# Performance work log

Measured on AMD Instinct MI355X. Metric: run time of the kernel, lower is better.

## Reference

```python
import jax, jax.numpy as jnp
import numpy as np

EPS = 1e-5

def _rmsnorm(x, g):
    xf = x.astype(jnp.float32)
    rms = jnp.sqrt(jnp.mean(xf * xf + EPS, axis=-1, keepdims=True))
    return (xf / rms * g).astype(x.dtype)

def setup_inputs() -> dict:
    key = jax.random.key(0)
    ks = jax.random.split(key, 10)
    B, S, D, H, F = 2, 2048, 1024, 16, 4096
    s = 0.02
    return {
        "x": jax.random.normal(ks[0], (B, S, D), jnp.float32),
        "g1": jnp.ones((D,), jnp.float32),
        "wq": jax.random.normal(ks[1], (D, D), jnp.float32) * s,
        "wk": jax.random.normal(ks[2], (D, D), jnp.float32) * s,
        "wv": jax.random.normal(ks[3], (D, D), jnp.float32) * s,
        "wo": jax.random.normal(ks[4], (D, D), jnp.float32) * s,
        "g2": jnp.ones((D,), jnp.float32),
        "w1": jax.random.normal(ks[5], (F, D), jnp.float32) * s,
        "w2": jax.random.normal(ks[6], (D, F), jnp.float32) * s,
        "w3": jax.random.normal(ks[7], (F, D), jnp.float32) * s,
    }

def reference(x, g1, wq, wk, wv, wo, g2, w1, w2, w3):
    B, S, D = x.shape
    H = 16
    hd = D // H
    # --- attention sublayer ---
    xn = _rmsnorm(x, g1)
    q = jnp.einsum('bsd,ed->bse', xn, wq).reshape(B, S, H, hd).transpose(0, 2, 1, 3)
    k = jnp.einsum('bsd,ed->bse', xn, wk).reshape(B, S, H, hd).transpose(0, 2, 1, 3)
    v = jnp.einsum('bsd,ed->bse', xn, wv).reshape(B, S, H, hd).transpose(0, 2, 1, 3)
    scores = jnp.einsum('bhqd,bhkd->bhqk', q, k) / jnp.sqrt(jnp.float32(hd))
    mask = jnp.tril(jnp.ones((S, S), bool))  # causal
    neg = jnp.finfo(scores.dtype).min
    scores = jnp.where(mask[None, None], scores, neg)
    probs = jax.nn.softmax(scores, axis=-1)
    o = jnp.einsum('bhqk,bhkd->bhqd', probs, v)
    o = o.transpose(0, 2, 1, 3).reshape(B, S, D)
    attn_out = jnp.einsum('bsv,dv->bsd', o, wo)
    h = x + attn_out
    # --- SwiGLU sublayer ---
    hn = _rmsnorm(h, g2)
    p1 = jnp.einsum('fd,bsd->bsf', w1, hn)
    p3 = jnp.einsum('fd,bsd->bsf', w3, hn)
    ffn = jnp.einsum('df,bsf->bsd', w2, jax.nn.silu(p1) * p3)
    return h + ffn
```

## Files before the change

### kernel.cpp

```cpp
#include <hip/hip_runtime.h>

typedef __attribute__((ext_vector_type(8))) short short8;
typedef __attribute__((ext_vector_type(4))) float f32x4;

__device__ __forceinline__ unsigned short f2b(float f) {
  union { float f; unsigned u; } v; v.f = f;
  unsigned r = v.u + 0x7fffu + ((v.u >> 16) & 1u);
  return (unsigned short)(r >> 16);
}
__device__ __forceinline__ float b2f(unsigned short b) {
  union { unsigned u; float f; } v; v.u = ((unsigned)b) << 16; return v.f;
}

__device__ __forceinline__ void gload_lds16(const void* g, void* l) {
  __builtin_amdgcn_global_load_lds(
      (const __attribute__((address_space(1))) void*)g,
      (__attribute__((address_space(3))) void*)l, 16, 0, 0);
}

__global__ __launch_bounds__(256) void cvt_k(const float* __restrict__ s,
                                             unsigned short* __restrict__ d, int n4) {
  int i = blockIdx.x * 256 + threadIdx.x;
  if (i >= n4) return;
  float4 v = ((const float4*)s)[i];
  ushort4 o;
  o.x = f2b(v.x); o.y = f2b(v.y); o.z = f2b(v.z); o.w = f2b(v.w);
  ((ushort4*)d)[i] = o;
}

__global__ __launch_bounds__(256) void rmsnorm_k(const float* __restrict__ x,
                                                 const float* __restrict__ g,
                                                 unsigned short* __restrict__ out) {
  const int row = blockIdx.x, tid = threadIdx.x;
  const float4 v = ((const float4*)(x + (size_t)row * 1024))[tid];
  float ss = v.x*v.x + v.y*v.y + v.z*v.z + v.w*v.w;
  #pragma unroll
  for (int d = 32; d > 0; d >>= 1) ss += __shfl_down(ss, d);
  __shared__ float red[4];
  if ((tid & 63) == 0) red[tid >> 6] = ss;
  __syncthreads();
  const float tot = red[0] + red[1] + red[2] + red[3];
  const float sc = rsqrtf(tot * (1.0f/1024.0f) + 1e-5f);
  const float4 gg = ((const float4*)g)[tid];
  ushort4 o;
  o.x = f2b(v.x * sc * gg.x); o.y = f2b(v.y * sc * gg.y);
  o.z = f2b(v.z * sc * gg.z); o.w = f2b(v.w * sc * gg.w);
  ((ushort4*)(out + (size_t)row * 1024))[tid] = o;
}

__global__ __launch_bounds__(256) void gate_k(unsigned short* __restrict__ p13) {
  const size_t i = (size_t)blockIdx.x * 256 + threadIdx.x;
  const int r = (int)(i >> 9);
  const int fc = ((int)i & 511) * 8;
  unsigned short* p1 = p13 + (size_t)r * 8192 + fc;
  const unsigned short* p3 = p13 + (size_t)r * 8192 + 4096 + fc;
  ushort4 a0 = ((const ushort4*)p1)[0], a1 = ((const ushort4*)p1)[1];
  ushort4 b0 = ((const ushort4*)p3)[0], b1 = ((const ushort4*)p3)[1];
  unsigned short va[8] = {a0.x,a0.y,a0.z,a0.w,a1.x,a1.y,a1.z,a1.w};
  unsigned short vb[8] = {b0.x,b0.y,b0.z,b0.w,b1.x,b1.y,b1.z,b1.w};
  unsigned short vo[8];
  #pragma unroll
  for (int j = 0; j < 8; ++j) {
    float f1 = b2f(va[j]), f3 = b2f(vb[j]);
    float s = f1 / (1.0f + __expf(-f1));
    vo[j] = f2b(s * f3);
  }
  ushort4 o0 = {vo[0],vo[1],vo[2],vo[3]}, o1 = {vo[4],vo[5],vo[6],vo[7]};
  ((ushort4*)p1)[0] = o0; ((ushort4*)p1)[1] = o1;
}

template<int EPI>
__global__ __launch_bounds__(256) void gemm_bt(
    const unsigned short* __restrict__ A, const unsigned short* __restrict__ W,
    int N, int K, int lda,
    unsigned short* __restrict__ Cb, const float* __restrict__ res,
    float* __restrict__ Cf, int ldc)
{
  __shared__ unsigned short sA[4096];
  __shared__ unsigned short sB[4096];
  const int tid = threadIdx.x;
  const int w = tid >> 6, l = tid & 63;
  const int l15 = l & 15, l4 = l >> 4;
  const int bm = blockIdx.y * 128, bn = blockIdx.x * 128;
  const int wm = (w >> 1) * 64, wn = (w & 1) * 64;
  const int c0 = w * 128 + l;
  const int ra0 = c0 >> 2,        ka0 = (c0 & 3) * 8;
  const int ra1 = (c0 + 64) >> 2, ka1 = ((c0 + 64) & 3) * 8;
  const unsigned short* Ar0 = A + (size_t)(bm + ra0) * lda + ka0;
  const unsigned short* Ar1 = A + (size_t)(bm + ra1) * lda + ka1;
  const unsigned short* Wr0 = W + (size_t)(bn + ra0) * K + ka0;
  const unsigned short* Wr1 = W + (size_t)(bn + ra1) * K + ka1;
  f32x4 acc[4][4];
  const f32x4 z4 = {0.f, 0.f, 0.f, 0.f};
  #pragma unroll
  for (int i = 0; i < 4; ++i)
    #pragma unroll
    for (int j = 0; j < 4; ++j) acc[i][j] = z4;

  for (int kt = 0; kt < K; kt += 32) {
    gload_lds16(Ar0 + kt, &sA[w * 1024]);
    gload_lds16(Ar1 + kt, &sA[w * 1024 + 512]);
    gload_lds16(Wr0 + kt, &sB[w * 1024]);
    gload_lds16(Wr1 + kt, &sB[w * 1024 + 512]);
    __syncthreads();
    short8 af[4], bf[4];
    #pragma unroll
    for (int mi = 0; mi < 4; ++mi)
      af[mi] = *(const short8*)&sA[(wm + mi*16 + l15)*32 + l4*8];
    #pragma unroll
    for (int ni = 0; ni < 4; ++ni)
      bf[ni] = *(const short8*)&sB[(wn + ni*16 + l15)*32 + l4*8];
    #pragma unroll
    for (int mi = 0; mi < 4; ++mi)
      #pragma unroll
      for (int ni = 0; ni < 4; ++ni)
        acc[mi][ni] = __builtin_amdgcn_mfma_f32_16x16x32_bf16(af[mi], bf[ni], acc[mi][ni], 0, 0, 0);
    __syncthreads();
  }
  #pragma unroll
  for (int mi = 0; mi < 4; ++mi)
    #pragma unroll
    for (int ni = 0; ni < 4; ++ni) {
      const int row0 = bm + wm + mi*16 + l4*4;
      const int col  = bn + wn + ni*16 + l15;
      #pragma unroll
      for (int r = 0; r < 4; ++r) {
        const float v = acc[mi][ni][r];
        if (EPI == 0) {
          Cb[(size_t)(row0 + r) * ldc + col] = f2b(v);
        } else {
          const size_t o = (size_t)(row0 + r) * ldc + col;
          Cf[o] = res[o] + v;
        }
      }
    }
}

__global__ __launch_bounds__(512, 2) void gemm256_bt(
    const unsigned short* __restrict__ A, const unsigned short* __restrict__ W,
    int K, int lda, unsigned short* __restrict__ Cb, int ldc, int nbx)
{
  __shared__ unsigned short sA[4][8192];
  __shared__ unsigned short sB[4][8192];
  const int tid = threadIdx.x;
  const int w = tid >> 6, l = tid & 63;
  const int l15 = l & 15, l4 = l >> 4;
  const int nwg = nbx * gridDim.y;
  const int flat = blockIdx.y * nbx + blockIdx.x;
  const int q8 = nwg >> 3;
  const int sw = (flat & 7) * q8 + (flat >> 3);
  const int bm = (sw / nbx) * 256, bn = (sw % nbx) * 256;

  int rowl[2], coll[2];
  #pragma unroll
  for (int i = 0; i < 2; ++i) {
    const int g = w * 128 + i * 64 + l;
    const int s = g >> 6, j = g & 63;
    const int r = j >> 2, c8 = (j & 3) * 8;
    rowl[i] = s * 16 + r;
    coll[i] = c8 ^ ((r & 8) << 1);
  }
  const unsigned short* As0 = A + (size_t)(bm + rowl[0]) * lda + coll[0];
  const unsigned short* As1 = A + (size_t)(bm + rowl[1]) * lda + coll[1];
  const unsigned short* Ws0 = W + (size_t)(bn + rowl[0]) * K + coll[0];
  const unsigned short* Ws1 = W + (size_t)(bn + rowl[1]) * K + coll[1];
  const int d0 = w * 1024, d1 = w * 1024 + 512;

  const int swzr = (l4 * 8) ^ ((l15 & 8) << 1);
  const int aoff = (w >> 2) * 4096 + l15 * 32 + swzr;
  const int boff = (w & 3) * 2048 + l15 * 32 + swzr;

  f32x4 acc[8][4];
  const f32x4 z4 = {0.f, 0.f, 0.f, 0.f};
  #pragma unroll
  for (int i = 0; i < 8; ++i)
    #pragma unroll
    for (int j = 0; j < 4; ++j) acc[i][j] = z4;

  const int NT = K >> 5;
  #pragma unroll
  for (int p = 0; p < 3; ++p) {
    const int ko = p * 32;
    gload_lds16(As0 + ko, &sA[p][d0]);
    gload_lds16(As1 + ko, &sA[p][d1]);
    gload_lds16(Ws0 + ko, &sB[p][d0]);
    gload_lds16(Ws1 + ko, &sB[p][d1]);
  }
  asm volatile("s_waitcnt vmcnt(8)" ::: "memory");
  __builtin_amdgcn_s_barrier();

  for (int t = 0; t < NT; ++t) {
    const unsigned short* a_ = sA[t & 3];
    const unsigned short* b_ = sB[t & 3];
    const bool st = (t + 3 < NT);
    const int nb = (t + 3) & 3;
    const int ko = (t + 3) * 32;
    short8 bfr[4], afr[4];
    #pragma unroll
    for (int ni = 0; ni < 4; ++ni) bfr[ni] = *(const short8*)&b_[boff + ni * 512];
    #pragma unroll
    for (int mi = 0; mi < 4; ++mi) afr[mi] = *(const short8*)&a_[aoff + mi * 512];
    if (st) { gload_lds16(As0 + ko, &sA[nb][d0]); gload_lds16(Ws0 + ko, &sB[nb][d0]); }
    __builtin_amdgcn_s_barrier();
    asm volatile("s_waitcnt lgkmcnt(0)" ::: "memory");
    __builtin_amdgcn_sched_barrier(0);
    __builtin_amdgcn_s_setprio(1);
    #pragma unroll
    for (int mi = 0; mi < 4; ++mi)
      #pragma unroll
      for (int ni = 0; ni < 4; ++ni)
        acc[mi][ni] = __builtin_amdgcn_mfma_f32_16x16x32_bf16(bfr[ni], afr[mi], acc[mi][ni], 0, 0, 0);
    __builtin_amdgcn_s_setprio(0);
    __builtin_amdgcn_s_barrier();
    #pragma unroll
    for (int mi = 0; mi < 4; ++mi) afr[mi] = *(const short8*)&a_[aoff + (mi + 4) * 512];
    if (st) { gload_lds16(As1 + ko, &sA[nb][d1]); gload_lds16(Ws1 + ko, &sB[nb][d1]); }
    __builtin_amdgcn_s_barrier();
    asm volatile("s_waitcnt lgkmcnt(0)" ::: "memory");
    __builtin_amdgcn_sched_barrier(0);
    __builtin_amdgcn_s_setprio(1);
    #pragma unroll
    for (int mi = 0; mi < 4; ++mi)
      #pragma unroll
      for (int ni = 0; ni < 4; ++ni)
        acc[mi + 4][ni] = __builtin_amdgcn_mfma_f32_16x16x32_bf16(bfr[ni], afr[mi], acc[mi + 4][ni], 0, 0, 0);
    __builtin_amdgcn_s_setprio(0);
    if (t < NT - 3)       asm volatile("s_waitcnt vmcnt(8)" ::: "memory");
    else if (t == NT - 3) asm volatile("s_waitcnt vmcnt(4)" ::: "memory");
    else                  asm volatile("s_waitcnt vmcnt(0)" ::: "memory");
    __builtin_amdgcn_s_barrier();
  }
  #pragma unroll
  for (int mi = 0; mi < 8; ++mi) {
    const int row = bm + (w >> 2) * 128 + mi * 16 + l15;
    #pragma unroll
    for (int ni = 0; ni < 4; ++ni) {
      const int col = bn + (w & 3) * 64 + ni * 16 + l4 * 4;
      ushort4 o = { f2b(acc[mi][ni][0]), f2b(acc[mi][ni][1]),
                    f2b(acc[mi][ni][2]), f2b(acc[mi][ni][3]) };
      *(ushort4*)&Cb[(size_t)row * ldc + col] = o;
    }
  }
}

__global__ __launch_bounds__(256) void vtrans_k(const unsigned short* __restrict__ QKV,
                                                unsigned short* __restrict__ VT) {
  __shared__ unsigned short sT[4096];
  const int st = blockIdx.x, dt = blockIdx.y, b = blockIdx.z;
  const int tid = threadIdx.x;
  #pragma unroll
  for (int half = 0; half < 2; ++half) {
    const int c = tid + half * 256;
    const int r = c >> 3;
    const int ch = c & 7;
    const unsigned short* src =
        QKV + (size_t)(b*2048 + st*64 + r) * 3072 + 2048 + dt*64 + ch*8;
    short8 v = *(const short8*)src;
    *(short8*)&sT[r*64 + ((ch ^ ((r >> 3) & 7)) * 8)] = v;
  }
  __syncthreads();
  #pragma unroll
  for (int half = 0; half < 2; ++half) {
    const int c = tid + half * 256;
    const int od = c >> 3;
    const int oc = c & 7;
    unsigned short tmp[8];
    #pragma unroll
    for (int j = 0; j < 8; ++j) {
      const int srow = oc*8 + j;
      const int chunk = (od >> 3) ^ ((srow >> 3) & 7);
      tmp[j] = sT[srow*64 + chunk*8 + (od & 7)];
    }
    *(short8*)&VT[(size_t)(b*1024 + dt*64 + od) * 2048 + st*64 + oc*8] = *(short8*)tmp;
  }
}

__global__ __launch_bounds__(256) void attn_k(const unsigned short* __restrict__ QKV,
                                              const unsigned short* __restrict__ VT,
                                              unsigned short* __restrict__ Ob)
{
  const int LDQ = 3072;
  const int b = blockIdx.y >> 4, h = blockIdx.y & 15;
  const int qb = (15 - (int)blockIdx.x) * 128;
  const int tid = threadIdx.x;
  const int w = tid >> 6, l = tid & 63;
  const int l15 = l & 15, l4 = l >> 4;
  const int qw = qb + w * 32;
  const unsigned short* Qg  = QKV + (size_t)(b * 2048) * LDQ + h * 64;
  const unsigned short* Kg  = Qg + 1024;
  const unsigned short* VTg = VT + (size_t)(b * 1024 + h * 64) * 2048;

  __shared__ unsigned short sK[2][4096];
  __shared__ unsigned short sVT[2][4096];
  __shared__ unsigned short sP[4][2304];

  short8 qf[2][2];
  #pragma unroll
  for (int qt = 0; qt < 2; ++qt)
    #pragma unroll
    for (int hc = 0; hc < 2; ++hc)
      qf[qt][hc] = *(const short8*)&Qg[(size_t)(qw + qt*16 + l15) * LDQ + hc*32 + l4*8];

  const int rc0 = tid >> 3;
  const int ch0 = (tid & 7) ^ (rc0 & 7);
  const int rc1 = rc0 + 32;
  const unsigned short* Ks0 = Kg  + (size_t)rc0 * LDQ  + ch0 * 8;
  const unsigned short* Ks1 = Kg  + (size_t)rc1 * LDQ  + ch0 * 8;
  const unsigned short* Vs0 = VTg + (size_t)rc0 * 2048 + ch0 * 8;
  const unsigned short* Vs1 = VTg + (size_t)rc1 * 2048 + ch0 * 8;
  const int wun0 = w * 512;
  const int wun1 = 2048 + w * 512;

  f32x4 accO[2][4];
  float m_run[2][4], l_run[2][4];
  const f32x4 z4 = {0.f,0.f,0.f,0.f};
  #pragma unroll
  for (int qt = 0; qt < 2; ++qt) {
    #pragma unroll
    for (int dt = 0; dt < 4; ++dt) accO[qt][dt] = z4;
    #pragma unroll
    for (int r = 0; r < 4; ++r) { m_run[qt][r] = -1e30f; l_run[qt][r] = 0.f; }
  }

  const int ntB = (qb >> 6) + 2;
#define ASTAGE(buf, t) do { \
    const size_t ko = (size_t)(t) * 64 * LDQ; const int vo = (t) * 64; \
    gload_lds16(Ks0 + ko, &sK[buf][wun0]); \
    gload_lds16(Ks1 + ko, &sK[buf][wun1]); \
    gload_lds16(Vs0 + vo, &sVT[buf][wun0]); \
    gload_lds16(Vs1 + vo, &sVT[buf][wun1]); } while (0)

  ASTAGE(0, 0);
  __syncthreads();
  int cur = 0;
  for (int t = 0; t < ntB; ++t) {
    if (t + 1 < ntB) ASTAGE(cur ^ 1, t + 1);
    const int kv = t * 64;
    if (kv <= qw + 31) {
      const unsigned short* Kb = sK[cur];
      const unsigned short* Vb = sVT[cur];
      const int lim = qw + 31 - kv;
      f32x4 sAcc[2][4];
      #pragma unroll
      for (int qt = 0; qt < 2; ++qt)
        #pragma unroll
        for (int nt = 0; nt < 4; ++nt) sAcc[qt][nt] = z4;
      #pragma unroll
      for (int nt = 0; nt < 4; ++nt) {
        if (nt * 16 <= lim) {
          const int krow = nt*16 + l15;
          const short8 kf0 = *(const short8*)&Kb[krow*64 + ((l4 ^ (krow & 7)) * 8)];
          const short8 kf1 = *(const short8*)&Kb[krow*64 + (((4 + l4) ^ (krow & 7)) * 8)];
          #pragma unroll
          for (int qt = 0; qt < 2; ++qt) {
            sAcc[qt][nt] = __builtin_amdgcn_mfma_f32_16x16x32_bf16(qf[qt][0], kf0, sAcc[qt][nt], 0,0,0);
            sAcc[qt][nt] = __builtin_amdgcn_mfma_f32_16x16x32_bf16(qf[qt][1], kf1, sAcc[qt][nt], 0,0,0);
          }
        }
      }
      const bool bound = (kv + 63 > qw);
      #pragma unroll
      for (int qt = 0; qt < 2; ++qt) {
        float fac[4]; bool resc_any = false;
        #pragma unroll
        for (int r = 0; r < 4; ++r) {
          float sv[4];
          #pragma unroll
          for (int nt = 0; nt < 4; ++nt)
            sv[nt] = (nt * 16 <= lim) ? sAcc[qt][nt][r] * 0.125f : -1e30f;
          if (bound) {
            const int row = qt*16 + l4*4 + r;
            #pragma unroll
            for (int nt = 0; nt < 4; ++nt)
              if (kv + nt*16 + l15 > qw + row) sv[nt] = -1e30f;
          }
          float mx = fmaxf(fmaxf(sv[0], sv[1]), fmaxf(sv[2], sv[3]));
          mx = fmaxf(mx, __shfl_xor(mx, 1));
          mx = fmaxf(mx, __shfl_xor(mx, 2));
          mx = fmaxf(mx, __shfl_xor(mx, 4));
          mx = fmaxf(mx, __shfl_xor(mx, 8));
          const float mo = m_run[qt][r];
          const bool resc = mx > mo + 8.0f;
          const float mn = resc ? mx : mo;
          const float f = resc ? __expf(mo - mn) : 1.0f;
          fac[r] = f; resc_any |= resc;
          const float p0 = __expf(sv[0]-mn), p1 = __expf(sv[1]-mn);
          const float p2 = __expf(sv[2]-mn), p3 = __expf(sv[3]-mn);
          float rs = (p0+p1)+(p2+p3);
          rs += __shfl_xor(rs,1); rs += __shfl_xor(rs,2);
          rs += __shfl_xor(rs,4); rs += __shfl_xor(rs,8);
          l_run[qt][r] = l_run[qt][r]*f + rs;
          m_run[qt][r] = mn;
          const int prow = qt*16 + l4*4 + r;
          sP[w][prow*72      + l15] = f2b(p0);
          sP[w][prow*72 + 16 + l15] = f2b(p1);
          sP[w][prow*72 + 32 + l15] = f2b(p2);
          sP[w][prow*72 + 48 + l15] = f2b(p3);
        }
        if (__any(resc_any)) {
          #pragma unroll
          for (int dt = 0; dt < 4; ++dt)
            #pragma unroll
            for (int r = 0; r < 4; ++r)
              accO[qt][dt][r] *= fac[r];
        }
      }
      short8 pf[2][2];
      #pragma unroll
      for (int qt = 0; qt < 2; ++qt)
        #pragma unroll
        for (int kc = 0; kc < 2; ++kc)
          pf[qt][kc] = *(const short8*)&sP[w][(qt*16 + l15)*72 + kc*32 + l4*8];
      #pragma unroll
      for (int dt = 0; dt < 4; ++dt) {
        const int vrow = dt*16 + l15;
        const short8 vf0 = *(const short8*)&Vb[vrow*64 + ((l4 ^ (vrow & 7)) * 8)];
        const short8 vf1 = *(const short8*)&Vb[vrow*64 + (((4 + l4) ^ (vrow & 7)) * 8)];
        #pragma unroll
        for (int qt = 0; qt < 2; ++qt) {
          accO[qt][dt] = __builtin_amdgcn_mfma_f32_16x16x32_bf16(pf[qt][0], vf0, accO[qt][dt], 0,0,0);
          accO[qt][dt] = __builtin_amdgcn_mfma_f32_16x16x32_bf16(pf[qt][1], vf1, accO[qt][dt], 0,0,0);
        }
      }
    }
    __syncthreads();
    cur ^= 1;
  }
  #pragma unroll
  for (int qt = 0; qt < 2; ++qt)
    #pragma unroll
    for (int dt = 0; dt < 4; ++dt)
      #pragma unroll
      for (int r = 0; r < 4; ++r) {
        const int row = qw + qt*16 + l4*4 + r;
        const float ov = accO[qt][dt][r] / l_run[qt][r];
        Ob[(size_t)(b*2048 + row) * 1024 + h*64 + dt*16 + l15] = f2b(ov);
      }
}

extern "C" void kernel_launch(void* const* d_in, const int* in_sizes, int n_in,
                              void* d_out, int out_size, void* d_ws, size_t ws_size,
                              hipStream_t stream) {
  const float* x  = (const float*)d_in[0];
  const float* g1 = (const float*)d_in[1];
  const float* wq = (const float*)d_in[2];
  const float* wk = (const float*)d_in[3];
  const float* wv = (const float*)d_in[4];
  const float* wo = (const float*)d_in[5];
  const float* g2 = (const float*)d_in[6];
  const float* w1 = (const float*)d_in[7];
  const float* w2 = (const float*)d_in[8];
  const float* w3 = (const float*)d_in[9];
  float* out = (float*)d_out;
  char* ws = (char*)d_ws;
  (void)in_sizes; (void)n_in; (void)out_size; (void)ws_size;

  unsigned short* Wqkv = (unsigned short*)(ws + 0);
  unsigned short* Wo   = (unsigned short*)(ws + 6291456);
  unsigned short* W13  = (unsigned short*)(ws + 8388608);
  unsigned short* W2   = (unsigned short*)(ws + 25165824);
  unsigned short* XN   = (unsigned short*)(ws + 33554432);
  unsigned short* QKV  = (unsigned short*)(ws + 41943040);
  unsigned short* OB   = (unsigned short*)(ws + 67108864);
  unsigned short* VTb  = (unsigned short*)(ws + 75497472);
  unsigned short* P13  = (unsigned short*)(ws + 41943040);
  float*          H    = (float*)(ws + 109051904);

  cvt_k<<<1024, 256, 0, stream>>>(wq, Wqkv,             262144);
  cvt_k<<<1024, 256, 0, stream>>>(wk, Wqkv + 1048576,   262144);
  cvt_k<<<1024, 256, 0, stream>>>(wv, Wqkv + 2097152,   262144);
  cvt_k<<<1024, 256, 0, stream>>>(wo, Wo,               262144);
  cvt_k<<<4096, 256, 0, stream>>>(w1, W13,             1048576);
  cvt_k<<<4096, 256, 0, stream>>>(w3, W13 + 4194304,   1048576);
  cvt_k<<<4096, 256, 0, stream>>>(w2, W2,              1048576);

  rmsnorm_k<<<4096, 256, 0, stream>>>(x, g1, XN);
  gemm256_bt<<<dim3(12, 16), 512, 0, stream>>>(XN, Wqkv, 1024, 1024, QKV, 3072, 12);
  vtrans_k<<<dim3(32, 16, 2), 256, 0, stream>>>(QKV, VTb);
  attn_k<<<dim3(16, 32), 256, 0, stream>>>(QKV, VTb, OB);
  gemm_bt<1><<<dim3(8, 32), 256, 0, stream>>>(OB, Wo, 1024, 1024, 1024,
                                              nullptr, x, H, 1024);
  rmsnorm_k<<<4096, 256, 0, stream>>>(H, g2, XN);
  gemm256_bt<<<dim3(32, 16), 512, 0, stream>>>(XN, W13, 1024, 1024, P13, 8192, 32);
  gate_k<<<8192, 256, 0, stream>>>(P13);
  gemm_bt<1><<<dim3(8, 32), 256, 0, stream>>>(P13, W2, 1024, 4096, 8192,
                                              nullptr, H, out, 1024);
}
```

Measured before the change: 569.1 us.

## Halve attention query tile to 64 rows, use exp2 softmax and MFMA priority

The attention kernel now gives each block 64 query rows instead of 128, so each wave handles 16 rows and the grid doubles to 1024 blocks. This improves load balance across the causal triangle and cuts per-wave register use, at the cost of loading each K/V tile twice as often. Softmax now folds log2(e) into the scale and uses exp2f, and s_setprio raises wave priority around the MFMA loops.

```diff
diff --git a/kernel.cpp b/kernel.cpp
--- a/kernel.cpp
+++ b/kernel.cpp
@@ -280,26 +280,25 @@
                                               unsigned short* __restrict__ Ob)
 {
   const int LDQ = 3072;
+  const float C2 = 0.125f * 1.44269504088896f;
   const int b = blockIdx.y >> 4, h = blockIdx.y & 15;
-  const int qb = (15 - (int)blockIdx.x) * 128;
+  const int qb = (31 - (int)blockIdx.x) * 64;
   const int tid = threadIdx.x;
   const int w = tid >> 6, l = tid & 63;
   const int l15 = l & 15, l4 = l >> 4;
-  const int qw = qb + w * 32;
+  const int qw = qb + w * 16;
   const unsigned short* Qg  = QKV + (size_t)(b * 2048) * LDQ + h * 64;
   const unsigned short* Kg  = Qg + 1024;
   const unsigned short* VTg = VT + (size_t)(b * 1024 + h * 64) * 2048;
 
   __shared__ unsigned short sK[2][4096];
   __shared__ unsigned short sVT[2][4096];
-  __shared__ unsigned short sP[4][2304];
-
-  short8 qf[2][2];
-  #pragma unroll
-  for (int qt = 0; qt < 2; ++qt)
-    #pragma unroll
-    for (int hc = 0; hc < 2; ++hc)
-      qf[qt][hc] = *(const short8*)&Qg[(size_t)(qw + qt*16 + l15) * LDQ + hc*32 + l4*8];
+  __shared__ unsigned short sP[4][1152];
+
+  short8 qf[2];
+  #pragma unroll
+  for (int hc = 0; hc < 2; ++hc)
+    qf[hc] = *(const short8*)&Qg[(size_t)(qw + l15) * LDQ + hc*32 + l4*8];
 
   const int rc0 = tid >> 3;
   const int ch0 = (tid & 7) ^ (rc0 & 7);
@@ -311,18 +310,15 @@
   const int wun0 = w * 512;
   const int wun1 = 2048 + w * 512;
 
-  f32x4 accO[2][4];
-  float m_run[2][4], l_run[2][4];
+  f32x4 accO[4];
+  float m_run[4], l_run[4];
   const f32x4 z4 = {0.f,0.f,0.f,0.f};
   #pragma unroll
-  for (int qt = 0; qt < 2; ++qt) {
-    #pragma unroll
-    for (int dt = 0; dt < 4; ++dt) accO[qt][dt] = z4;
-    #pragma unroll
-    for (int r = 0; r < 4; ++r) { m_run[qt][r] = -1e30f; l_run[qt][r] = 0.f; }
-  }
-
-  const int ntB = (qb >> 6) + 2;
+  for (int dt = 0; dt < 4; ++dt) accO[dt] = z4;
+  #pragma unroll
+  for (int r = 0; r < 4; ++r) { m_run[r] = -1e30f; l_run[r] = 0.f; }
+
+  const int ntB = (qb >> 6) + 1;
 #define ASTAGE(buf, t) do { \
     const size_t ko = (size_t)(t) * 64 * LDQ; const int vo = (t) * 64; \
     gload_lds16(Ks0 + ko, &sK[buf][wun0]); \
@@ -336,106 +332,93 @@
   for (int t = 0; t < ntB; ++t) {
     if (t + 1 < ntB) ASTAGE(cur ^ 1, t + 1);
     const int kv = t * 64;
-    if (kv <= qw + 31) {
-      const unsigned short* Kb = sK[cur];
-      const unsigned short* Vb = sVT[cur];
-      const int lim = qw + 31 - kv;
-      f32x4 sAcc[2][4];
-      #pragma unroll
-      for (int qt = 0; qt < 2; ++qt)
+    const unsigned short* Kb = sK[cur];
+    const unsigned short* Vb = sVT[cur];
+    const int lim = qw + 15 - kv;
+    f32x4 sAcc[4];
+    #pragma unroll
+    for (int nt = 0; nt < 4; ++nt) sAcc[nt] = z4;
+    __builtin_amdgcn_s_setprio(1);
+    #pragma unroll
+    for (int nt = 0; nt < 4; ++nt) {
+      if (nt * 16 <= lim) {
+        const int krow = nt*16 + l15;
+        const short8 kf0 = *(const short8*)&Kb[krow*64 + ((l4 ^ (krow & 7)) * 8)];
+        const short8 kf1 = *(const short8*)&Kb[krow*64 + (((4 + l4) ^ (krow & 7)) * 8)];
+        sAcc[nt] = __builtin_amdgcn_mfma_f32_16x16x32_bf16(qf[0], kf0, sAcc[nt], 0,0,0);
+        sAcc[nt] = __builtin_amdgcn_mfma_f32_16x16x32_bf16(qf[1], kf1, sAcc[nt], 0,0,0);
+      }
+    }
+    __builtin_amdgcn_s_setprio(0);
+    const bool bound = (kv + 63 > qw);
+    float fac[4]; bool resc_any = false;
+    #pragma unroll
+    for (int r = 0; r < 4; ++r) {
+      float sv[4];
+      #pragma unroll
+      for (int nt = 0; nt < 4; ++nt)
+        sv[nt] = (nt * 16 <= lim) ? sAcc[nt][r] * C2 : -1e30f;
+      if (bound) {
+        const int row = l4*4 + r;
         #pragma unroll
-        for (int nt = 0; nt < 4; ++nt) sAcc[qt][nt] = z4;
-      #pragma unroll
-      for (int nt = 0; nt < 4; ++nt) {
-        if (nt * 16 <= lim) {
-          const int krow = nt*16 + l15;
-          const short8 kf0 = *(const short8*)&Kb[krow*64 + ((l4 ^ (krow & 7)) * 8)];
-          const short8 kf1 = *(const short8*)&Kb[krow*64 + (((4 + l4) ^ (krow & 7)) * 8)];
-          #pragma unroll
-          for (int qt = 0; qt < 2; ++qt) {
-            sAcc[qt][nt] = __builtin_amdgcn_mfma_f32_16x16x32_bf16(qf[qt][0], kf0, sAcc[qt][nt], 0,0,0);
-            sAcc[qt][nt] = __builtin_amdgcn_mfma_f32_16x16x32_bf16(qf[qt][1], kf1, sAcc[qt][nt], 0,0,0);
-          }
-        }
+        for (int nt = 0; nt < 4; ++nt)
+          if (kv + nt*16 + l15 > qw + row) sv[nt] = -1e30f;
       }
-      const bool bound = (kv + 63 > qw);
-      #pragma unroll
-      for (int qt = 0; qt < 2; ++qt) {
-        float fac[4]; bool resc_any = false;
+      float mx = fmaxf(fmaxf(sv[0], sv[1]), fmaxf(sv[2], sv[3]));
+      mx = fmaxf(mx, __shfl_xor(mx, 1));
+      mx = fmaxf(mx, __shfl_xor(mx, 2));
+      mx = fmaxf(mx, __shfl_xor(mx, 4));
+      mx = fmaxf(mx, __shfl_xor(mx, 8));
+      const float mo = m_run[r];
+      const bool resc = mx > mo + 8.0f;
+      const float mn = resc ? mx : mo;
+      const float f = resc ? exp2f(mo - mn) : 1.0f;
+      fac[r] = f; resc_any |= resc;
+      const float p0 = exp2f(sv[0]-mn), p1 = exp2f(sv[1]-mn);
+      const float p2 = exp2f(sv[2]-mn), p3 = exp2f(sv[3]-mn);
+      float rs = (p0+p1)+(p2+p3);
+      rs += __shfl_xor(rs,1); rs += __shfl_xor(rs,2);
+      rs += __shfl_xor(rs,4); rs += __shfl_xor(rs,8);
+      l_run[r] = l_run[r]*f + rs;
+      m_run[r] = mn;
+      const int prow = l4*4 + r;
+      sP[w][prow*72      + l15] = f2b(p0);
+      sP[w][prow*72 + 16 + l15] = f2b(p1);
+      sP[w][prow*72 + 32 + l15] = f2b(p2);
+      sP[w][prow*72 + 48 + l15] = f2b(p3);
+    }
+    if (__any(resc_any)) {
+      #pragma unroll
+      for (int dt = 0; dt < 4; ++dt)
         #pragma unroll
-        for (int r = 0; r < 4; ++r) {
-          float sv[4];
-          #pragma unroll
-          for (int nt = 0; nt < 4; ++nt)
-            sv[nt] = (nt * 16 <= lim) ? sAcc[qt][nt][r] * 0.125f : -1e30f;
-          if (bound) {
-            const int row = qt*16 + l4*4 + r;
-            #pragma unroll
-            for (int nt = 0; nt < 4; ++nt)
-              if (kv + nt*16 + l15 > qw + row) sv[nt] = -1e30f;
-          }
-          float mx = fmaxf(fmaxf(sv[0], sv[1]), fmaxf(sv[2], sv[3]));
-          mx = fmaxf(mx, __shfl_xor(mx, 1));
-          mx = fmaxf(mx, __shfl_xor(mx, 2));
-          mx = fmaxf(mx, __shfl_xor(mx, 4));
-          mx = fmaxf(mx, __shfl_xor(mx, 8));
-          const float mo = m_run[qt][r];
-          const bool resc = mx > mo + 8.0f;
-          const float mn = resc ? mx : mo;
-          const float f = resc ? __expf(mo - mn) : 1.0f;
-          fac[r] = f; resc_any |= resc;
-          const float p0 = __expf(sv[0]-mn), p1 = __expf(sv[1]-mn);
-          const float p2 = __expf(sv[2]-mn), p3 = __expf(sv[3]-mn);
-          float rs = (p0+p1)+(p2+p3);
-          rs += __shfl_xor(rs,1); rs += __shfl_xor(rs,2);
-          rs += __shfl_xor(rs,4); rs += __shfl_xor(rs,8);
-          l_run[qt][r] = l_run[qt][r]*f + rs;
-          m_run[qt][r] = mn;
-          const int prow = qt*16 + l4*4 + r;
-          sP[w][prow*72      + l15] = f2b(p0);
-          sP[w][prow*72 + 16 + l15] = f2b(p1);
-          sP[w][prow*72 + 32 + l15] = f2b(p2);
-          sP[w][prow*72 + 48 + l15] = f2b(p3);
-        }
-        if (__any(resc_any)) {
-          #pragma unroll
-          for (int dt = 0; dt < 4; ++dt)
-            #pragma unroll
-            for (int r = 0; r < 4; ++r)
-              accO[qt][dt][r] *= fac[r];
-        }
-      }
-      short8 pf[2][2];
-      #pragma unroll
-      for (int qt = 0; qt < 2; ++qt)
-        #pragma unroll
-        for (int kc = 0; kc < 2; ++kc)
-          pf[qt][kc] = *(const short8*)&sP[w][(qt*16 + l15)*72 + kc*32 + l4*8];
-      #pragma unroll
-      for (int dt = 0; dt < 4; ++dt) {
-        const int vrow = dt*16 + l15;
-        const short8 vf0 = *(const short8*)&Vb[vrow*64 + ((l4 ^ (vrow & 7)) * 8)];
-        const short8 vf1 = *(const short8*)&Vb[vrow*64 + (((4 + l4) ^ (vrow & 7)) * 8)];
-        #pragma unroll
-        for (int qt = 0; qt < 2; ++qt) {
-          accO[qt][dt] = __builtin_amdgcn_mfma_f32_16x16x32_bf16(pf[qt][0], vf0, accO[qt][dt], 0,0,0);
-          accO[qt][dt] = __builtin_amdgcn_mfma_f32_16x16x32_bf16(pf[qt][1], vf1, accO[qt][dt], 0,0,0);
-        }
-      }
-    }
+        for (int r = 0; r < 4; ++r)
+          accO[dt][r] *= fac[r];
+    }
+    short8 pf[2];
+    #pragma unroll
+    for (int kc = 0; kc < 2; ++kc)
+      pf[kc] = *(const short8*)&sP[w][l15*72 + kc*32 + l4*8];
+    __builtin_amdgcn_s_setprio(1);
+    #pragma unroll
+    for (int dt = 0; dt < 4; ++dt) {
+      const int vrow = dt*16 + l15;
+      const short8 vf0 = *(const short8*)&Vb[vrow*64 + ((l4 ^ (vrow & 7)) * 8)];
+      const short8 vf1 = *(const short8*)&Vb[vrow*64 + (((4 + l4) ^ (vrow & 7)) * 8)];
+      accO[dt] = __builtin_amdgcn_mfma_f32_16x16x32_bf16(pf[0], vf0, accO[dt], 0,0,0);
+      accO[dt] = __builtin_amdgcn_mfma_f32_16x16x32_bf16(pf[1], vf1, accO[dt], 0,0,0);
+    }
+    __builtin_amdgcn_s_setprio(0);
     __syncthreads();
     cur ^= 1;
   }
   #pragma unroll
-  for (int qt = 0; qt < 2; ++qt)
-    #pragma unroll
-    for (int dt = 0; dt < 4; ++dt)
-      #pragma unroll
-      for (int r = 0; r < 4; ++r) {
-        const int row = qw + qt*16 + l4*4 + r;
-        const float ov = accO[qt][dt][r] / l_run[qt][r];
-        Ob[(size_t)(b*2048 + row) * 1024 + h*64 + dt*16 + l15] = f2b(ov);
-      }
+  for (int dt = 0; dt < 4; ++dt)
+    #pragma unroll
+    for (int r = 0; r < 4; ++r) {
+      const int row = qw + l4*4 + r;
+      const float ov = accO[dt][r] / l_run[r];
+      Ob[(size_t)(b*2048 + row) * 1024 + h*64 + dt*16 + l15] = f2b(ov);
+    }
 }
 
 extern "C" void kernel_launch(void* const* d_in, const int* in_sizes, int n_in,
@@ -477,7 +460,7 @@
   rmsnorm_k<<<4096, 256, 0, stream>>>(x, g1, XN);
   gemm256_bt<<<dim3(12, 16), 512, 0, stream>>>(XN, Wqkv, 1024, 1024, QKV, 3072, 12);
   vtrans_k<<<dim3(32, 16, 2), 256, 0, stream>>>(QKV, VTb);
-  attn_k<<<dim3(16, 32), 256, 0, stream>>>(QKV, VTb, OB);
+  attn_k<<<dim3(32, 32), 256, 0, stream>>>(QKV, VTb, OB);
   gemm_bt<1><<<dim3(8, 32), 256, 0, stream>>>(OB, Wo, 1024, 1024, 1024,
                                               nullptr, x, H, 1024);
   rmsnorm_k<<<4096, 256, 0, stream>>>(H, g2, XN);
```

Result: slower. 602.9 us (+5.9%).
